# Performance work log

Hardware: AMD Instinct MI355X
Metric: run time of the kernel (lower is better)

Reference implementation:

```python
import jax, jax.numpy as jnp
import numpy as np

TAB_DIM = 6
C = 64
B, X, Y, Z = 2, 64, 64, 64
EPS = float(np.finfo(np.float32).eps)


def _gauss_1d(mu, sigma, size):
    # mu, sigma: (B, C) -> mask (B, C, size)
    coords = jnp.arange(size, dtype=jnp.float32)  # (size,)
    mu = mu * (size / 2.0) + (size / 2.0) - 0.5
    sigma = sigma * 3.5 + EPS
    d = (coords[None, None, :] - mu[:, :, None]) / sigma[:, :, None]
    return jnp.exp(-0.5 * d * d)


def _frob(t):
    return jnp.sqrt(jnp.sum(t * t))


def setup_inputs() -> dict:
    key = jax.random.key(0)
    ks = jax.random.split(key, 10)
    h = C // 2
    def lin(k, fan_in, fan_out):
        bound = 1.0 / np.sqrt(fan_in)
        kw, kb = jax.random.split(k)
        w = jax.random.uniform(kw, (fan_out, fan_in), jnp.float32, -bound, bound)
        b = jax.random.uniform(kb, (fan_out,), jnp.float32, -bound, bound)
        return w, b
    w1, b1 = lin(ks[0], TAB_DIM, h)
    w2, b2 = lin(ks[1], h, h)
    wp, bp = lin(ks[2], h, 5 * C)
    ws, bs = lin(ks[3], h, 3 * C)
    x = jax.random.normal(ks[4], (B, C, X, Y, Z), jnp.float32)
    tab = jax.random.normal(ks[5], (B, TAB_DIM), jnp.float32)
    return {"x": x, "tab": tab, "w1": w1, "b1": b1, "w2": w2, "b2": b2,
            "wp": wp, "bp": bp, "ws": ws, "bs": bs}


def reference(x, tab, w1, b1, w2, b2, wp, bp, ws, bs):
    # hypernetwork (tiny MLPs)
    emb = jnp.tanh(tab @ w1.T + b1)
    emb = jnp.tanh(emb @ w2.T + b2)
    p = emb @ wp.T + bp                     # (B, 5C)
    s = jax.nn.sigmoid(emb @ ws.T + bs)     # (B, 3C)
    scale = p[..., :C]
    shift = p[..., C:2 * C]
    mu_a = jnp.tanh(p[..., 2 * C:3 * C])
    mu_b = jnp.tanh(p[..., 3 * C:4 * C])
    mu_c = jnp.tanh(p[..., 4 * C:])
    sigma_a = s[..., :C]
    sigma_b = s[..., C:2 * C]
    sigma_c = s[..., 2 * C:]

    l2 = _frob(scale) + _frob(shift) + _frob(sigma_a) + _frob(sigma_b) + _frob(sigma_c)

    _, _, sx, sy, sz = x.shape
    gx = _gauss_1d(mu_a, sigma_a, sx)  # (B, C, X)
    gy = _gauss_1d(mu_b, sigma_b, sy)  # (B, C, Y)
    gz = _gauss_1d(mu_c, sigma_c, sz)  # (B, C, Z)

    # rank-1 outer product over X,Y,Z == the chained matmuls in torch
    a = gx[:, :, :, None, None] * gy[:, :, None, :, None] * gz[:, :, None, None, :]

    out = (1.0 - scale)[:, :, None, None, None] * x * a + shift[:, :, None, None, None]
    return out, l2
```

## Files before the change

### kernel.cpp

```cpp
#include <hip/hip_runtime.h>
#include <math.h>

#define EPSF 1.1920929e-07f

typedef float f4 __attribute__((ext_vector_type(4)));

__device__ __forceinline__ float sigmoid_fast(float v) {
    return 1.0f / (1.0f + __expf(-v));
}
__device__ __forceinline__ float tanh_fast(float x) {
    float ax = fabsf(x);
    float e  = __expf(-2.0f * ax);
    float t  = (1.0f - e) / (1.0f + e);
    return copysignf(t, x);
}
__device__ __forceinline__ float gauss_fast(float i, float m, float sg) {
    float d = (i - m) / sg;
    return __expf(-0.5f * d * d);
}

__global__ void __launch_bounds__(256) fused_kernel(
        const float* __restrict__ xin, const float* __restrict__ tab,
        const float* __restrict__ w1,  const float* __restrict__ b1,
        const float* __restrict__ w2,  const float* __restrict__ b2,
        const float* __restrict__ wp,  const float* __restrict__ bp,
        const float* __restrict__ wsg, const float* __restrict__ bsg,
        float* __restrict__ out, int out_last)
{
    __shared__ float emb1[2][32];
    __shared__ float emb2[2][32];
    __shared__ float head[8];
    __shared__ float gys[64];
    __shared__ f4    gz4[16];
    __shared__ float pv_sh, sh_sh;

    const int blk = blockIdx.x;
    const int bc  = blk >> 6;
    const int xi  = blk & 63;
    const int b   = bc >> 6;
    const int c   = bc & 63;
    const int tid = threadIdx.x;

    const f4* x4 = (const f4*)(xin + (size_t)blk * 4096);
    f4*       o4 = (f4*)(out + (size_t)blk * 4096);
    f4 x0 = __builtin_nontemporal_load(&x4[tid]);
    f4 x1 = __builtin_nontemporal_load(&x4[tid + 256]);
    f4 x2 = __builtin_nontemporal_load(&x4[tid + 512]);
    f4 x3 = __builtin_nontemporal_load(&x4[tid + 768]);

    if (tid < 64) {
        int bb = tid >> 5, j = tid & 31;
        float acc = b1[j];
        #pragma unroll
        for (int k = 0; k < 6; ++k) acc += tab[bb * 6 + k] * w1[j * 6 + k];
        emb1[bb][j] = tanh_fast(acc);
    }
    __syncthreads();

    if (tid < 64) {
        int bb = tid >> 5, j = tid & 31;
        const f4* wr = (const f4*)(w2 + j * 32);
        float acc = b2[j];
        #pragma unroll
        for (int q = 0; q < 8; ++q) {
            f4 wv = wr[q];
            acc += wv.x * emb1[bb][q * 4 + 0] + wv.y * emb1[bb][q * 4 + 1]
                 + wv.z * emb1[bb][q * 4 + 2] + wv.w * emb1[bb][q * 4 + 3];
        }
        emb2[bb][j] = tanh_fast(acc);
    }
    __syncthreads();

    if (tid < 8) {
        const float* W  = (tid < 5) ? wp  : wsg;
        const float* Bv = (tid < 5) ? bp  : bsg;
        int row = ((tid < 5) ? tid : (tid - 5)) * 64 + c;
        const f4* wr = (const f4*)(W + row * 32);
        float acc = Bv[row];
        #pragma unroll
        for (int q = 0; q < 8; ++q) {
            f4 wv = wr[q];
            acc += wv.x * emb2[b][q * 4 + 0] + wv.y * emb2[b][q * 4 + 1]
                 + wv.z * emb2[b][q * 4 + 2] + wv.w * emb2[b][q * 4 + 3];
        }
        head[tid] = acc;
    }
    __syncthreads();

    if (tid < 64) {
        float m  = tanh_fast(head[3]) * 32.0f + 31.5f;
        float sg = sigmoid_fast(head[6]) * 3.5f + EPSF;
        gys[tid] = gauss_fast((float)tid, m, sg);
    } else if (tid < 128) {
        int i = tid - 64;
        float m  = tanh_fast(head[4]) * 32.0f + 31.5f;
        float sg = sigmoid_fast(head[7]) * 3.5f + EPSF;
        ((float*)gz4)[i] = gauss_fast((float)i, m, sg);
    } else if (tid == 128) {
        float m  = tanh_fast(head[2]) * 32.0f + 31.5f;
        float sg = sigmoid_fast(head[5]) * 3.5f + EPSF;
        pv_sh = (1.0f - head[0]) * gauss_fast((float)xi, m, sg);
        sh_sh = head[1];
    }

    if (blk == 0) {
        __shared__ float sq[5][128];
        for (int t = tid; t < 640; t += 256) {
            int q = t / 128, r = t % 128;
            int bb = r >> 6, cc = r & 63;
            const float* W  = (q < 2) ? wp  : wsg;
            const float* Bv = (q < 2) ? bp  : bsg;
            int row = ((q < 2) ? q : (q - 2)) * 64 + cc;
            const f4* wr = (const f4*)(W + row * 32);
            float acc = Bv[row];
            #pragma unroll
            for (int u = 0; u < 8; ++u) {
                f4 wv = wr[u];
                acc += wv.x * emb2[bb][u * 4 + 0] + wv.y * emb2[bb][u * 4 + 1]
                     + wv.z * emb2[bb][u * 4 + 2] + wv.w * emb2[bb][u * 4 + 3];
            }
            if (q >= 2) acc = sigmoid_fast(acc);
            sq[q][r] = acc * acc;
        }
        __syncthreads();
        if (tid == 0) {
            float tot = 0.0f;
            for (int q = 0; q < 5; ++q) {
                float ssum = 0.0f;
                for (int i = 0; i < 128; ++i) ssum += sq[q][i];
                tot += sqrtf(ssum);
            }
            out[out_last] = tot;
        }
    }
    __syncthreads();

    const float pv = pv_sh;
    const float sh = sh_sh;
    const int   yb = tid >> 4;
    const f4    vz = gz4[tid & 15];
    const float s0 = pv * gys[yb];
    const float s1 = pv * gys[yb + 16];
    const float s2 = pv * gys[yb + 32];
    const float s3 = pv * gys[yb + 48];
    const f4 shv = {sh, sh, sh, sh};

    __builtin_nontemporal_store((vz * x0) * s0 + shv, &o4[tid]);
    __builtin_nontemporal_store((vz * x1) * s1 + shv, &o4[tid + 256]);
    __builtin_nontemporal_store((vz * x2) * s2 + shv, &o4[tid + 512]);
    __builtin_nontemporal_store((vz * x3) * s3 + shv, &o4[tid + 768]);
}

extern "C" void kernel_launch(void* const* d_in, const int* in_sizes, int n_in,
                              void* d_out, int out_size, void* d_ws, size_t ws_size,
                              hipStream_t stream)
{
    const float* x   = (const float*)d_in[0];
    const float* tab = (const float*)d_in[1];
    const float* w1  = (const float*)d_in[2];
    const float* b1  = (const float*)d_in[3];
    const float* w2  = (const float*)d_in[4];
    const float* b2  = (const float*)d_in[5];
    const float* wp  = (const float*)d_in[6];
    const float* bp  = (const float*)d_in[7];
    const float* wsg = (const float*)d_in[8];
    const float* bsg = (const float*)d_in[9];

    float* out = (float*)d_out;

    fused_kernel<<<2 * 64 * 64, 256, 0, stream>>>(
        x, tab, w1, b1, w2, b2, wp, bp, wsg, bsg, out, out_size - 1);
}
```

Baseline: 52.29 us.

## Replace shared-memory hypernetwork with per-wavefront shuffles, drop all block barriers

```diff
diff --git a/kernel.cpp b/kernel.cpp
--- a/kernel.cpp
+++ b/kernel.cpp
@@ -19,7 +19,7 @@
     return __expf(-0.5f * d * d);
 }
 
-__global__ void __launch_bounds__(256) fused_kernel(
+__global__ void __launch_bounds__(256, 8) fused_kernel(
         const float* __restrict__ xin, const float* __restrict__ tab,
         const float* __restrict__ w1,  const float* __restrict__ b1,
         const float* __restrict__ w2,  const float* __restrict__ b2,
@@ -27,19 +27,13 @@
         const float* __restrict__ wsg, const float* __restrict__ bsg,
         float* __restrict__ out, int out_last)
 {
-    __shared__ float emb1[2][32];
-    __shared__ float emb2[2][32];
-    __shared__ float head[8];
-    __shared__ float gys[64];
-    __shared__ f4    gz4[16];
-    __shared__ float pv_sh, sh_sh;
-
-    const int blk = blockIdx.x;
-    const int bc  = blk >> 6;
-    const int xi  = blk & 63;
-    const int b   = bc >> 6;
-    const int c   = bc & 63;
-    const int tid = threadIdx.x;
+    const int tid  = threadIdx.x;
+    const int lane = tid & 63;
+    const int blk  = blockIdx.x;
+    const int bc   = blk >> 6;
+    const int xi   = blk & 63;
+    const int b    = bc >> 6;
+    const int c    = bc & 63;
 
     const f4* x4 = (const f4*)(xin + (size_t)blk * 4096);
     f4*       o4 = (f4*)(out + (size_t)blk * 4096);
@@ -48,107 +42,115 @@
     f4 x2 = __builtin_nontemporal_load(&x4[tid + 512]);
     f4 x3 = __builtin_nontemporal_load(&x4[tid + 768]);
 
-    if (tid < 64) {
-        int bb = tid >> 5, j = tid & 31;
+    const int bb = lane >> 5;
+    const int j  = lane & 31;
+    float e1;
+    {
         float acc = b1[j];
         #pragma unroll
         for (int k = 0; k < 6; ++k) acc += tab[bb * 6 + k] * w1[j * 6 + k];
-        emb1[bb][j] = tanh_fast(acc);
+        e1 = tanh_fast(acc);
     }
-    __syncthreads();
 
-    if (tid < 64) {
-        int bb = tid >> 5, j = tid & 31;
+    float e2;
+    {
         const f4* wr = (const f4*)(w2 + j * 32);
         float acc = b2[j];
         #pragma unroll
         for (int q = 0; q < 8; ++q) {
             f4 wv = wr[q];
-            acc += wv.x * emb1[bb][q * 4 + 0] + wv.y * emb1[bb][q * 4 + 1]
-                 + wv.z * emb1[bb][q * 4 + 2] + wv.w * emb1[bb][q * 4 + 3];
+            int base = (lane & 32) + q * 4;
+            acc += wv.x * __shfl(e1, base + 0)
+                 + wv.y * __shfl(e1, base + 1)
+                 + wv.z * __shfl(e1, base + 2)
+                 + wv.w * __shfl(e1, base + 3);
         }
-        emb2[bb][j] = tanh_fast(acc);
+        e2 = tanh_fast(acc);
     }
-    __syncthreads();
 
-    if (tid < 8) {
-        const float* W  = (tid < 5) ? wp  : wsg;
-        const float* Bv = (tid < 5) ? bp  : bsg;
-        int row = ((tid < 5) ? tid : (tid - 5)) * 64 + c;
-        const f4* wr = (const f4*)(W + row * 32);
-        float acc = Bv[row];
+    float h;
+    {
+        const int hidx = lane & 7;
+        const float* Wh = (hidx < 5) ? wp : wsg;
+        const float* Bh = (hidx < 5) ? bp : bsg;
+        const int hrow  = ((hidx < 5) ? hidx : hidx - 5) * 64 + c;
+        const f4* wr = (const f4*)(Wh + hrow * 32);
+        h = Bh[hrow];
         #pragma unroll
         for (int q = 0; q < 8; ++q) {
             f4 wv = wr[q];
-            acc += wv.x * emb2[b][q * 4 + 0] + wv.y * emb2[b][q * 4 + 1]
-                 + wv.z * emb2[b][q * 4 + 2] + wv.w * emb2[b][q * 4 + 3];
+            int base = b * 32 + q * 4;
+            h += wv.x * __shfl(e2, base + 0)
+               + wv.y * __shfl(e2, base + 1)
+               + wv.z * __shfl(e2, base + 2)
+               + wv.w * __shfl(e2, base + 3);
         }
-        head[tid] = acc;
     }
-    __syncthreads();
+    const float h0 = __shfl(h, 0), h1 = __shfl(h, 1), h2 = __shfl(h, 2),
+                h3 = __shfl(h, 3), h4 = __shfl(h, 4), h5 = __shfl(h, 5),
+                h6 = __shfl(h, 6), h7 = __shfl(h, 7);
 
-    if (tid < 64) {
-        float m  = tanh_fast(head[3]) * 32.0f + 31.5f;
-        float sg = sigmoid_fast(head[6]) * 3.5f + EPSF;
-        gys[tid] = gauss_fast((float)tid, m, sg);
-    } else if (tid < 128) {
-        int i = tid - 64;
-        float m  = tanh_fast(head[4]) * 32.0f + 31.5f;
-        float sg = sigmoid_fast(head[7]) * 3.5f + EPSF;
-        ((float*)gz4)[i] = gauss_fast((float)i, m, sg);
-    } else if (tid == 128) {
-        float m  = tanh_fast(head[2]) * 32.0f + 31.5f;
-        float sg = sigmoid_fast(head[5]) * 3.5f + EPSF;
-        pv_sh = (1.0f - head[0]) * gauss_fast((float)xi, m, sg);
-        sh_sh = head[1];
+    const float m_a = tanh_fast(h2) * 32.0f + 31.5f;
+    const float m_b = tanh_fast(h3) * 32.0f + 31.5f;
+    const float m_c = tanh_fast(h4) * 32.0f + 31.5f;
+    const float s_a = sigmoid_fast(h5) * 3.5f + EPSF;
+    const float s_b = sigmoid_fast(h6) * 3.5f + EPSF;
+    const float s_c = sigmoid_fast(h7) * 3.5f + EPSF;
+
+    const float pv = (1.0f - h0) * gauss_fast((float)xi, m_a, s_a);
+    const float sh = h1;
+
+    const int yb = tid >> 4;
+    const int z0 = (tid & 15) << 2;
+    f4 vz;
+    vz.x = gauss_fast((float)(z0 + 0), m_c, s_c);
+    vz.y = gauss_fast((float)(z0 + 1), m_c, s_c);
+    vz.z = gauss_fast((float)(z0 + 2), m_c, s_c);
+    vz.w = gauss_fast((float)(z0 + 3), m_c, s_c);
+
+    const f4 cw0 = vz * (pv * gauss_fast((float)(yb +  0), m_b, s_b));
+    const f4 cw1 = vz * (pv * gauss_fast((float)(yb + 16), m_b, s_b));
+    const f4 cw2 = vz * (pv * gauss_fast((float)(yb + 32), m_b, s_b));
+    const f4 cw3 = vz * (pv * gauss_fast((float)(yb + 48), m_b, s_b));
+    const f4 shv = {sh, sh, sh, sh};
+
+    if (blk == 0 && tid < 64) {
+        float tot = 0.0f;
+        #pragma unroll
+        for (int q = 0; q < 5; ++q) {
+            float ss = 0.0f;
+            #pragma unroll
+            for (int half = 0; half < 2; ++half) {
+                int rr  = half * 64 + lane;
+                int bbq = rr >> 6, cc = rr & 63;
+                const float* W  = (q < 2) ? wp  : wsg;
+                const float* Bv = (q < 2) ? bp  : bsg;
+                int row = ((q < 2) ? q : (q - 2)) * 64 + cc;
+                const f4* wr = (const f4*)(W + row * 32);
+                float a = Bv[row];
+                #pragma unroll
+                for (int u = 0; u < 8; ++u) {
+                    f4 wv = wr[u];
+                    int base = bbq * 32 + u * 4;
+                    a += wv.x * __shfl(e2, base + 0)
+                       + wv.y * __shfl(e2, base + 1)
+                       + wv.z * __shfl(e2, base + 2)
+                       + wv.w * __shfl(e2, base + 3);
+                }
+                if (q >= 2) a = sigmoid_fast(a);
+                ss += a * a;
+            }
+            #pragma unroll
+            for (int off = 32; off > 0; off >>= 1) ss += __shfl_xor(ss, off);
+            tot += sqrtf(ss);
+        }
+        if (lane == 0) out[out_last] = tot;
     }
 
-    if (blk == 0) {
-        __shared__ float sq[5][128];
-        for (int t = tid; t < 640; t += 256) {
-            int q = t / 128, r = t % 128;
-            int bb = r >> 6, cc = r & 63;
-            const float* W  = (q < 2) ? wp  : wsg;
-            const float* Bv = (q < 2) ? bp  : bsg;
-            int row = ((q < 2) ? q : (q - 2)) * 64 + cc;
-            const f4* wr = (const f4*)(W + row * 32);
-            float acc = Bv[row];
-            #pragma unroll
-            for (int u = 0; u < 8; ++u) {
-                f4 wv = wr[u];
-                acc += wv.x * emb2[bb][u * 4 + 0] + wv.y * emb2[bb][u * 4 + 1]
-                     + wv.z * emb2[bb][u * 4 + 2] + wv.w * emb2[bb][u * 4 + 3];
-            }
-            if (q >= 2) acc = sigmoid_fast(acc);
-            sq[q][r] = acc * acc;
-        }
-        __syncthreads();
-        if (tid == 0) {
-            float tot = 0.0f;
-            for (int q = 0; q < 5; ++q) {
-                float ssum = 0.0f;
-                for (int i = 0; i < 128; ++i) ssum += sq[q][i];
-                tot += sqrtf(ssum);
-            }
-            out[out_last] = tot;
-        }
-    }
-    __syncthreads();
-
-    const float pv = pv_sh;
-    const float sh = sh_sh;
-    const int   yb = tid >> 4;
-    const f4    vz = gz4[tid & 15];
-    const float s0 = pv * gys[yb];
-    const float s1 = pv * gys[yb + 16];
-    const float s2 = pv * gys[yb + 32];
-    const float s3 = pv * gys[yb + 48];
-    const f4 shv = {sh, sh, sh, sh};
-
-    __builtin_nontemporal_store((vz * x0) * s0 + shv, &o4[tid]);
-    __builtin_nontemporal_store((vz * x1) * s1 + shv, &o4[tid + 256]);
-    __builtin_nontemporal_store((vz * x2) * s2 + shv, &o4[tid + 512]);
-    __builtin_nontemporal_store((vz * x3) * s3 + shv, &o4[tid + 768]);
+    __builtin_nontemporal_store(cw0 * x0 + shv, &o4[tid]);
+    __builtin_nontemporal_store(cw1 * x1 + shv, &o4[tid + 256]);
+    __builtin_nontemporal_store(cw2 * x2 + shv, &o4[tid + 512]);
+    __builtin_nontemporal_store(cw3 * x3 + shv, &o4[tid + 768]);
 }
 
 extern "C" void kernel_launch(void* const* d_in, const int* in_sizes, int n_in,
```

New measurement: 120.6 us. 2.31x slower.
